# Performance work log

Measured on AMD Instinct MI355X. Metric: run time of the kernel, lower is better.

## Reference

```python
import jax, jax.numpy as jnp
import numpy as np

N_NODES = 100000
N_EDGES = 1600000
D_FEAT = 64
H1 = 16
H2 = 1


def setup_inputs() -> dict:
    key = jax.random.key(0)
    ks = jax.random.split(key, 8)
    x = jax.random.normal(ks[0], (N_NODES, D_FEAT), dtype=jnp.float32)
    edge_index = jax.random.randint(ks[1], (2, N_EDGES), 0, N_NODES, dtype=jnp.int64)
    s1 = 1.0 / np.sqrt(D_FEAT)
    s2 = 1.0 / np.sqrt(H1)
    Wl1 = jax.random.uniform(ks[2], (H1, D_FEAT), jnp.float32, -s1, s1)
    Wr1 = jax.random.uniform(ks[3], (H1, D_FEAT), jnp.float32, -s1, s1)
    b1 = jax.random.uniform(ks[4], (H1,), jnp.float32, -s1, s1)
    Wl2 = jax.random.uniform(ks[5], (H2, H1), jnp.float32, -s2, s2)
    Wr2 = jax.random.uniform(ks[6], (H2, H1), jnp.float32, -s2, s2)
    b2 = jax.random.uniform(ks[7], (H2,), jnp.float32, -s2, s2)
    return {"x": x, "edge_index": edge_index, "Wl1": Wl1, "Wr1": Wr1, "b1": b1,
            "Wl2": Wl2, "Wr2": Wr2, "b2": b2}


def _sage_conv(h, src, dst, Wl, Wr, b, n_nodes):
    # mean aggregation of source-node features onto destination nodes
    msg_sum = jax.ops.segment_sum(h[src], dst, num_segments=n_nodes)  # [N, d]
    cnt = jax.ops.segment_sum(jnp.ones((src.shape[0],), h.dtype), dst,
                              num_segments=n_nodes)  # [N]
    mean = msg_sum / jnp.maximum(cnt, 1.0)[:, None]
    # out = lin_l(mean_neighbors) + lin_r(self) + bias
    return mean @ Wl.T + h @ Wr.T + b


def reference(x, edge_index, Wl1, Wr1, b1, Wl2, Wr2, b2):
    src, dst = edge_index[0], edge_index[1]
    n = x.shape[0]
    h = jax.nn.relu(_sage_conv(x, src, dst, Wl1, Wr1, b1, n))
    # F.dropout(training=False) is identity at inference
    out = _sage_conv(h, src, dst, Wl2, Wr2, b2, n)
    return out
```

## Files before the change

kernel.cpp:

```cpp
#include <hip/hip_runtime.h>
#include <hip/hip_fp16.h>

#define H1F 16
#define BSH 8
#define BNODES 256
#define MAXBUCK 512
#define CAPSH 13
#define CAPB (1 << CAPSH)
#define SSH 10
#define TILE 4096
#define MAXPT 16

struct Params {
    const float* x;
    const float* Wl1; const float* Wr1; const float* b1;
    const float* Wl2; const float* Wr2; const float* b2;
    const int* ei;
    int* cur8;
    unsigned int* edge2;
    int* csr; int* offp; int* degv;
    __half* xl; float* xr; float* hl2; float* outp;
    float* out;
    int N, E, nPart, nProj, nbuck;
};

union SharedU {
    struct {
        int lhist[MAXBUCK];
        int lbase[MAXBUCK];
        int gbase[MAXBUCK];
        int wsum[8];
        unsigned int stage[TILE];
        unsigned short sbuck[TILE];
    } p;
    struct {
        float4 wl4[16][17];
        float4 wr4[16][17];
    } q;
};

__device__ __forceinline__ void do_part(const Params& P, int vb, SharedU& sh) {
    int t = threadIdx.x;
    int shard = vb & 7;
    sh.p.lhist[t] = 0;
    __syncthreads();

    int E = P.E;
    int e0 = vb * TILE;
    int eb = e0 + t * 8;

    int ss[8], dd[8];
    if (eb + 8 <= E) {
        int4 s0 = *(const int4*)(P.ei + eb);
        int4 s1 = *(const int4*)(P.ei + eb + 4);
        int4 d0 = *(const int4*)(P.ei + E + eb);
        int4 d1 = *(const int4*)(P.ei + E + eb + 4);
        ss[0]=s0.x; ss[1]=s0.y; ss[2]=s0.z; ss[3]=s0.w;
        ss[4]=s1.x; ss[5]=s1.y; ss[6]=s1.z; ss[7]=s1.w;
        dd[0]=d0.x; dd[1]=d0.y; dd[2]=d0.z; dd[3]=d0.w;
        dd[4]=d1.x; dd[5]=d1.y; dd[6]=d1.z; dd[7]=d1.w;
    } else {
#pragma unroll
        for (int k = 0; k < 8; ++k) {
            int e = eb + k;
            ss[k] = (e < E) ? P.ei[e] : -1;
            dd[k] = (e < E) ? P.ei[E + e] : 0;
        }
    }

    unsigned int pk[8];
    int rk[8], bk[8];
#pragma unroll
    for (int k = 0; k < 8; ++k) {
        if (ss[k] >= 0) {
            int b = dd[k] >> BSH;
            bk[k] = b;
            pk[k] = ((unsigned int)ss[k] << BSH) |
                    (unsigned int)(dd[k] & (BNODES - 1));
            rk[k] = atomicAdd(&sh.p.lhist[b], 1);
        } else {
            bk[k] = -1;
        }
    }
    __syncthreads();

    int cnt = E - e0; if (cnt > TILE) cnt = TILE;

    int v = sh.p.lhist[t];
    if (v > 0)
        sh.p.gbase[t] = (t << CAPSH) + (shard << SSH) +
                        atomicAdd(&P.cur8[shard * MAXBUCK + t], v);
    int lane = t & 63, wid = t >> 6;
    int s = v;
#pragma unroll
    for (int d = 1; d < 64; d <<= 1) {
        int u = __shfl_up(s, d);
        if (lane >= d) s += u;
    }
    if (lane == 63) sh.p.wsum[wid] = s;
    __syncthreads();
    int wofs = 0;
    for (int w = 0; w < wid; ++w) wofs += sh.p.wsum[w];
    sh.p.lbase[t] = wofs + s - v;
    __syncthreads();

#pragma unroll
    for (int k = 0; k < 8; ++k) {
        if (bk[k] >= 0) {
            int p = sh.p.lbase[bk[k]] + rk[k];
            sh.p.stage[p] = pk[k];
            sh.p.sbuck[p] = (unsigned short)bk[k];
        }
    }
    __syncthreads();

    for (int i = t; i < cnt; i += 512) {
        int b = sh.p.sbuck[i];
        int idx = sh.p.gbase[b] + (i - sh.p.lbase[b]);
        int shardEnd = (b << CAPSH) + ((shard + 1) << SSH);
        if (idx < shardEnd) P.edge2[idx] = sh.p.stage[i];
    }
}

__device__ __forceinline__ void do_proj(const Params& P, int pvb, SharedU& sh) {
    int t = threadIdx.x;
    if (t < 256) {
        sh.q.wl4[t >> 4][t & 15] = ((const float4*)P.Wl1)[t];
    } else {
        int u = t - 256;
        sh.q.wr4[u >> 4][u & 15] = ((const float4*)P.Wr1)[u];
    }
    __syncthreads();

    int f = t & 15;
    int nl = t >> 4;
    float bf = P.b1[f];
    const float4* x4 = (const float4*)P.x;

#pragma unroll
    for (int rep = 0; rep < 4; ++rep) {
        int gn = pvb * 128 + rep * 32 + nl;
        if (gn < P.N) {
            float al = 0.0f, ar = 0.0f;
#pragma unroll
            for (int k4 = 0; k4 < 16; ++k4) {
                float4 xv = x4[(size_t)gn * 16 + k4];
                float4 a = sh.q.wl4[f][k4];
                float4 b = sh.q.wr4[f][k4];
                al += xv.x * a.x + xv.y * a.y + xv.z * a.z + xv.w * a.w;
                ar += xv.x * b.x + xv.y * b.y + xv.z * b.z + xv.w * b.w;
            }
            P.xl[(size_t)gn * H1F + f] = __float2half(al);
            P.xr[(size_t)gn * H1F + f] = ar + bf;
        }
    }
}

__global__ __launch_bounds__(512) void kA(Params P) {
    __shared__ SharedU sh;
    int vb = blockIdx.x;
    if (vb < P.nPart) do_part(P, vb, sh);
    else do_proj(P, vb - P.nPart, sh);
}

__global__ __launch_bounds__(512) void kBC(Params P) {
    __shared__ int sorted[CAPB];
    __shared__ int hh[BNODES];
    __shared__ int ofs[BNODES];
    __shared__ int dgs[BNODES];
    __shared__ int wsum[4];

    int t = threadIdx.x;
    int b = blockIdx.x;
    int n0 = b << BSH;
    int e0 = b << CAPSH;

    if (t < BNODES) hh[t] = 0;
    __syncthreads();

    int cnt = 0;
    unsigned int rw[MAXPT];
#pragma unroll
    for (int s = 0; s < 8; ++s) {
        int c = P.cur8[s * MAXBUCK + b];
        if (c > (1 << SSH)) c = (1 << SSH);
        cnt += c;
        int base = e0 + (s << SSH);
#pragma unroll
        for (int k = 0; k < 2; ++k) {
            int idx = (k << 9) + t;
            rw[s * 2 + k] = (idx < c) ? P.edge2[base + idx] : 0xFFFFFFFFu;
        }
    }

#pragma unroll
    for (int k = 0; k < MAXPT; ++k)
        if (rw[k] != 0xFFFFFFFFu) atomicAdd(&hh[rw[k] & (BNODES - 1)], 1);
    __syncthreads();

    int lane = t & 63, wid = t >> 6;
    int v = 0, s = 0;
    if (t < BNODES) {
        v = hh[t];
        s = v;
#pragma unroll
        for (int d = 1; d < 64; d <<= 1) {
            int u = __shfl_up(s, d);
            if (lane >= d) s += u;
        }
        if (lane == 63) wsum[wid] = s;
    }
    __syncthreads();
    if (t < BNODES) {
        int wofs = 0;
        for (int w = 0; w < wid; ++w) wofs += wsum[w];
        int excl = wofs + s - v;
        ofs[t] = excl;
        dgs[t] = v;
        int gn = n0 + t;
        if (gn < P.N) {
            P.degv[gn] = v;
            P.offp[gn] = e0 + excl;
        }
        hh[t] = excl;
    }
    __syncthreads();

#pragma unroll
    for (int k = 0; k < MAXPT; ++k) {
        if (rw[k] != 0xFFFFFFFFu) {
            int d = (int)(rw[k] & (BNODES - 1));
            int pos = atomicAdd(&hh[d], 1);
            sorted[pos] = (int)(rw[k] >> BSH);
        }
    }
    __syncthreads();

    for (int i = t; i < cnt; i += 512) P.csr[e0 + i] = sorted[i];

    const __half2* xl2 = (const __half2*)P.xl;
    const float2* xr2 = (const float2*)P.xr;
    int l = t & 7;
    int nb = t >> 3;
    float2 wlv = ((const float2*)P.Wl2)[l];
    float2 wrv = ((const float2*)P.Wr2)[l];
    float bias2 = P.b2[0];

#pragma unroll
    for (int sub = 0; sub < 4; ++sub) {
        int nl = sub * 64 + nb;
        int node = n0 + nl;
        if (node < P.N) {
            int start = ofs[nl];
            int d = dgs[nl];
            float sx = 0.0f, sy = 0.0f;
            int j = 0;
            for (; j + 4 <= d; j += 4) {
                int s0 = sorted[start + j], s1 = sorted[start + j + 1];
                int s2 = sorted[start + j + 2], s3 = sorted[start + j + 3];
                float2 v0 = __half22float2(xl2[(size_t)s0 * 8 + l]);
                float2 v1 = __half22float2(xl2[(size_t)s1 * 8 + l]);
                float2 v2 = __half22float2(xl2[(size_t)s2 * 8 + l]);
                float2 v3 = __half22float2(xl2[(size_t)s3 * 8 + l]);
                sx += v0.x + v1.x + v2.x + v3.x;
                sy += v0.y + v1.y + v2.y + v3.y;
            }
            for (; j < d; ++j) {
                float2 vv = __half22float2(xl2[(size_t)sorted[start + j] * 8 + l]);
                sx += vv.x; sy += vv.y;
            }

            float inv = 1.0f / fmaxf((float)d, 1.0f);
            float2 xrv = xr2[(size_t)node * 8 + l];
            float h0 = fmaxf(sx * inv + xrv.x, 0.0f);
            float h1 = fmaxf(sy * inv + xrv.y, 0.0f);
            float pl = h0 * wlv.x + h1 * wlv.y;
            float pr = h0 * wrv.x + h1 * wrv.y;
#pragma unroll
            for (int off = 4; off; off >>= 1) {
                pl += __shfl_xor(pl, off);
                pr += __shfl_xor(pr, off);
            }
            if (l == 0) {
                P.hl2[node] = pl;
                P.outp[node] = pr + bias2;
            }
        }
    }
}

__global__ __launch_bounds__(512) void kD(Params P) {
    int g = blockIdx.x;
    int xcd = g & 7, r = g >> 3;
    int bi = r >> 1, k = r & 1;
    int b = bi * 8 + xcd;
    if (b >= P.nbuck) return;
    int t = threadIdx.x;
    int node = (b << BSH) + (k << 7) + (t >> 2);
    int l = t & 3;
    if (node >= P.N) return;

    int d = P.degv[node];
    const int* row = P.csr + P.offp[node];

    float s = 0.0f;
    for (int j = l; j < d; j += 4) s += P.hl2[row[j]];
    s += __shfl_xor(s, 1);
    s += __shfl_xor(s, 2);
    if (l == 0) P.out[node] = s / fmaxf((float)d, 1.0f) + P.outp[node];
}

extern "C" void kernel_launch(void* const* d_in, const int* in_sizes, int n_in,
                              void* d_out, int out_size, void* d_ws, size_t ws_size,
                              hipStream_t stream) {
    Params P;
    P.x   = (const float*)d_in[0];
    P.ei  = (const int*)d_in[1];
    P.Wl1 = (const float*)d_in[2];
    P.Wr1 = (const float*)d_in[3];
    P.b1  = (const float*)d_in[4];
    P.Wl2 = (const float*)d_in[5];
    P.Wr2 = (const float*)d_in[6];
    P.b2  = (const float*)d_in[7];
    P.out = (float*)d_out;

    P.N = in_sizes[0] / 64;
    P.E = in_sizes[1] / 2;
    P.nbuck = (P.N + BNODES - 1) >> BSH;
    P.nPart = (P.E + TILE - 1) / TILE;
    P.nProj = (P.N + 127) / 128;

    size_t win = (size_t)P.nbuck << CAPSH;
    P.cur8  = (int*)d_ws;
    P.edge2 = (unsigned int*)(P.cur8 + 8 * MAXBUCK);
    P.csr   = (int*)(P.edge2 + win);
    P.offp  = P.csr + win;
    P.degv  = P.offp + P.N;
    P.xl    = (__half*)(P.degv + P.N);
    P.xr    = (float*)(P.xl + (size_t)16 * P.N);
    P.hl2   = P.xr + (size_t)16 * P.N;
    P.outp  = P.hl2 + P.N;

    (void)hipMemsetAsync(P.cur8, 0, 8 * MAXBUCK * sizeof(int), stream);

    kA<<<P.nPart + P.nProj, 512, 0, stream>>>(P);
    kBC<<<P.nbuck, 512, 0, stream>>>(P);
    int gridD = 8 * ((P.nbuck + 7) / 8) * 2;
    kD<<<gridD, 512, 0, stream>>>(P);
}
```

Before: 68.01 us.

## Double partition tile, recompute ranks via second pass, write buckets per thread

The edge partition step now processes 8192 edges per block in two 4096-edge batches. It first builds a destination-bucket histogram, then reloads the edges and uses shared atomics on the prefix-summed bases to place each packed edge directly in the staging buffer. This drops the per-slot bucket array and the per-edge rank registers. The global write-out now has each thread copy its own bucket's run serially instead of striding over slots. The edge indices are read twice, and the per-thread serial copy gives uncoalesced, imbalanced global stores in exchange for fewer blocks and less per-block overhead.

```diff
diff --git a/kernel.cpp b/kernel.cpp
--- a/kernel.cpp
+++ b/kernel.cpp
@@ -8,7 +8,7 @@
 #define CAPSH 13
 #define CAPB (1 << CAPSH)
 #define SSH 10
-#define TILE 4096
+#define TILE 8192
 #define MAXPT 16
 
 struct Params {
@@ -31,7 +31,6 @@
         int gbase[MAXBUCK];
         int wsum[8];
         unsigned int stage[TILE];
-        unsigned short sbuck[TILE];
     } p;
     struct {
         float4 wl4[16][17];
@@ -47,44 +46,30 @@
 
     int E = P.E;
     int e0 = vb * TILE;
-    int eb = e0 + t * 8;
-
-    int ss[8], dd[8];
-    if (eb + 8 <= E) {
-        int4 s0 = *(const int4*)(P.ei + eb);
-        int4 s1 = *(const int4*)(P.ei + eb + 4);
-        int4 d0 = *(const int4*)(P.ei + E + eb);
-        int4 d1 = *(const int4*)(P.ei + E + eb + 4);
-        ss[0]=s0.x; ss[1]=s0.y; ss[2]=s0.z; ss[3]=s0.w;
-        ss[4]=s1.x; ss[5]=s1.y; ss[6]=s1.z; ss[7]=s1.w;
-        dd[0]=d0.x; dd[1]=d0.y; dd[2]=d0.z; dd[3]=d0.w;
-        dd[4]=d1.x; dd[5]=d1.y; dd[6]=d1.z; dd[7]=d1.w;
-    } else {
-#pragma unroll
-        for (int k = 0; k < 8; ++k) {
-            int e = eb + k;
-            ss[k] = (e < E) ? P.ei[e] : -1;
-            dd[k] = (e < E) ? P.ei[E + e] : 0;
-        }
-    }
-
-    unsigned int pk[8];
-    int rk[8], bk[8];
-#pragma unroll
-    for (int k = 0; k < 8; ++k) {
-        if (ss[k] >= 0) {
-            int b = dd[k] >> BSH;
-            bk[k] = b;
-            pk[k] = ((unsigned int)ss[k] << BSH) |
-                    (unsigned int)(dd[k] & (BNODES - 1));
-            rk[k] = atomicAdd(&sh.p.lhist[b], 1);
+
+#pragma unroll
+    for (int batch = 0; batch < 2; ++batch) {
+        int eb = e0 + batch * 4096 + t * 8;
+        if (eb + 8 <= E) {
+            int4 d0 = *(const int4*)(P.ei + E + eb);
+            int4 d1 = *(const int4*)(P.ei + E + eb + 4);
+            atomicAdd(&sh.p.lhist[d0.x >> BSH], 1);
+            atomicAdd(&sh.p.lhist[d0.y >> BSH], 1);
+            atomicAdd(&sh.p.lhist[d0.z >> BSH], 1);
+            atomicAdd(&sh.p.lhist[d0.w >> BSH], 1);
+            atomicAdd(&sh.p.lhist[d1.x >> BSH], 1);
+            atomicAdd(&sh.p.lhist[d1.y >> BSH], 1);
+            atomicAdd(&sh.p.lhist[d1.z >> BSH], 1);
+            atomicAdd(&sh.p.lhist[d1.w >> BSH], 1);
         } else {
-            bk[k] = -1;
-        }
-    }
-    __syncthreads();
-
-    int cnt = E - e0; if (cnt > TILE) cnt = TILE;
+#pragma unroll
+            for (int k = 0; k < 8; ++k) {
+                int e = eb + k;
+                if (e < E) atomicAdd(&sh.p.lhist[P.ei[E + e] >> BSH], 1);
+            }
+        }
+    }
+    __syncthreads();
 
     int v = sh.p.lhist[t];
     if (v > 0)
@@ -101,24 +86,55 @@
     __syncthreads();
     int wofs = 0;
     for (int w = 0; w < wid; ++w) wofs += sh.p.wsum[w];
-    sh.p.lbase[t] = wofs + s - v;
-    __syncthreads();
-
-#pragma unroll
-    for (int k = 0; k < 8; ++k) {
-        if (bk[k] >= 0) {
-            int p = sh.p.lbase[bk[k]] + rk[k];
-            sh.p.stage[p] = pk[k];
-            sh.p.sbuck[p] = (unsigned short)bk[k];
-        }
-    }
-    __syncthreads();
-
-    for (int i = t; i < cnt; i += 512) {
-        int b = sh.p.sbuck[i];
-        int idx = sh.p.gbase[b] + (i - sh.p.lbase[b]);
-        int shardEnd = (b << CAPSH) + ((shard + 1) << SSH);
-        if (idx < shardEnd) P.edge2[idx] = sh.p.stage[i];
+    int myBase = wofs + s - v;
+    sh.p.lbase[t] = myBase;
+    __syncthreads();
+    sh.p.lhist[t] = myBase;
+    __syncthreads();
+
+#pragma unroll
+    for (int batch = 0; batch < 2; ++batch) {
+        int eb = e0 + batch * 4096 + t * 8;
+        if (eb + 8 <= E) {
+            int4 s0 = *(const int4*)(P.ei + eb);
+            int4 s1 = *(const int4*)(P.ei + eb + 4);
+            int4 d0 = *(const int4*)(P.ei + E + eb);
+            int4 d1 = *(const int4*)(P.ei + E + eb + 4);
+            int ssv[8] = {s0.x, s0.y, s0.z, s0.w, s1.x, s1.y, s1.z, s1.w};
+            int ddv[8] = {d0.x, d0.y, d0.z, d0.w, d1.x, d1.y, d1.z, d1.w};
+#pragma unroll
+            for (int k = 0; k < 8; ++k) {
+                int b = ddv[k] >> BSH;
+                int pos = atomicAdd(&sh.p.lhist[b], 1);
+                sh.p.stage[pos] = ((unsigned int)ssv[k] << BSH) |
+                                  (unsigned int)(ddv[k] & (BNODES - 1));
+            }
+        } else {
+#pragma unroll
+            for (int k = 0; k < 8; ++k) {
+                int e = eb + k;
+                if (e < E) {
+                    int src = P.ei[e];
+                    int dst = P.ei[E + e];
+                    int b = dst >> BSH;
+                    int pos = atomicAdd(&sh.p.lhist[b], 1);
+                    sh.p.stage[pos] = ((unsigned int)src << BSH) |
+                                      (unsigned int)(dst & (BNODES - 1));
+                }
+            }
+        }
+    }
+    __syncthreads();
+
+    int lb = sh.p.lbase[t];
+    int cnt = sh.p.lhist[t] - lb;
+    if (cnt > 0) {
+        int gb = sh.p.gbase[t];
+        int subEnd = (t << CAPSH) + ((shard + 1) << SSH);
+        int jmax = subEnd - gb;
+        if (cnt < jmax) jmax = cnt;
+        for (int j = 0; j < jmax; ++j)
+            P.edge2[gb + j] = sh.p.stage[lb + j];
     }
 }
 
```

Result: faster. 65.24 us (-4.1%).
